# Optimization experiments

Measured on AMD Instinct MI355X. Metric: run time of the kernel, lower is better.

Reference implementation:

```python
import jax, jax.numpy as jnp
import numpy as np

B, C, H, W = 4, 512, 64, 64
C8 = C // 8


def setup_inputs() -> dict:
    key = jax.random.key(0)
    ks = jax.random.split(key, 8)
    s = 0.02
    return {
        "x": jax.random.normal(ks[0], (B, C, H, W), dtype=jnp.float32),
        "wq": jax.random.normal(ks[1], (C8, C), dtype=jnp.float32) * s,
        "bq": jax.random.normal(ks[2], (C8,), dtype=jnp.float32) * s,
        "wk": jax.random.normal(ks[3], (C8, C), dtype=jnp.float32) * s,
        "bk": jax.random.normal(ks[4], (C8,), dtype=jnp.float32) * s,
        "wv": jax.random.normal(ks[5], (C, C), dtype=jnp.float32) * s,
        "bv": jax.random.normal(ks[6], (C,), dtype=jnp.float32) * s,
        "gamma": jax.random.normal(ks[7], (1,), dtype=jnp.float32),
    }


def reference(x, wq, bq, wk, bk, wv, bv, gamma):
    b, c, h, w = x.shape
    # 1x1 convs == per-pixel linear projections
    q = jnp.einsum('bchw,oc->bohw', x, wq) + bq[None, :, None, None]  # [B,C8,H,W]
    k = jnp.einsum('bchw,oc->bohw', x, wk) + bk[None, :, None, None]  # [B,C8,H,W]
    v = jnp.einsum('bchw,oc->bohw', x, wv) + bv[None, :, None, None]  # [B,C,H,W]
    qf = q.reshape(b, c // 8, h * w)  # [B,C8,HW]
    kf = k.reshape(b, c // 8, h * w)  # [B,C8,HW]
    # energy[b,i,j] = q_i . k_j, viewed as [B,H,W,H,W]; softmax over last dim
    energy = jnp.einsum('bci,bcj->bij', qf, kf).reshape(b, h, w, h, w)
    attn = jax.nn.softmax(energy, axis=-1)  # [B,H,W,H2,W2]
    # torch: out = bmm(value, permute(0,1,3,2,4).view(B,HW,HW))
    # rows index (h,h2) into value's spatial grid; cols index output (w,w2)
    out = jnp.einsum('bchk,bhwkv->bcwv', v, attn)  # [B,C,H,W]
    return gamma * out + x
```

## Files before the change

kernel.cpp:

```cpp
#include <hip/hip_runtime.h>
#include <hip/hip_bf16.h>


typedef __bf16 bf16_t;
typedef __bf16 bf16x8 __attribute__((ext_vector_type(8)));
typedef __bf16 bf16x4 __attribute__((ext_vector_type(4)));
typedef float f32x4 __attribute__((ext_vector_type(4)));

#define HW_ 4096
#define CIN 512
#define CQ 64

__device__ __forceinline__ void gload16(const void* g, void* l) {
  __builtin_amdgcn_global_load_lds((const __attribute__((address_space(1))) void*)g,
                                   (__attribute__((address_space(3))) void*)l, 16, 0, 0);
}

__global__ __launch_bounds__(256) void k_wcat(const float* __restrict__ wq,
                                              const float* __restrict__ wk,
                                              const float* __restrict__ wv,
                                              bf16_t* __restrict__ Wcat) {
  int idx = (blockIdx.x * 256 + threadIdx.x) * 4;
  int row = idx >> 9, c = idx & 511;
  const float* src;
  if (row < 64)       src = wq + row * 512 + c;
  else if (row < 128) src = wk + (row - 64) * 512 + c;
  else                src = wv + (row - 128) * 512 + c;
  float4 v = *(const float4*)src;
  bf16x4 o = { (bf16_t)v.x, (bf16_t)v.y, (bf16_t)v.z, (bf16_t)v.w };
  *(bf16x4*)&Wcat[idx] = o;
}

__global__ __launch_bounds__(256) void k_prep(const float* __restrict__ x, bf16_t* __restrict__ xT) {
  __shared__ float tile[64][65];
  const int b = blockIdx.z;
  const int p0 = blockIdx.x * 64, c0 = blockIdx.y * 64;
  const float* xb = x + (size_t)b * CIN * HW_;
  bf16_t* xTb = xT + (size_t)b * HW_ * CIN;
  const int tid = threadIdx.x;
  const int r = tid >> 4, q = tid & 15;
#pragma unroll
  for (int i = 0; i < 4; ++i) {
    int lr = r + 16 * i;
    float4 v = *(const float4*)&xb[(size_t)(c0 + lr) * HW_ + p0 + q * 4];
    tile[lr][q * 4 + 0] = v.x; tile[lr][q * 4 + 1] = v.y;
    tile[lr][q * 4 + 2] = v.z; tile[lr][q * 4 + 3] = v.w;
  }
  __syncthreads();
#pragma unroll
  for (int i = 0; i < 4; ++i) {
    int pr = r + 16 * i;
    bf16x4 o;
    o[0] = (bf16_t)tile[q * 4 + 0][pr];
    o[1] = (bf16_t)tile[q * 4 + 1][pr];
    o[2] = (bf16_t)tile[q * 4 + 2][pr];
    o[3] = (bf16_t)tile[q * 4 + 3][pr];
    *(bf16x4*)&xTb[(size_t)(p0 + pr) * CIN + c0 + q * 4] = o;
  }
}

__global__ __launch_bounds__(256) void k_projqk(const bf16_t* __restrict__ Wcat,
                                                const bf16_t* __restrict__ xT,
                                                const float* __restrict__ bq,
                                                const float* __restrict__ bk,
                                                bf16_t* __restrict__ qfT,
                                                bf16_t* __restrict__ kfT) {
  __shared__ bf16_t As[128][64];
  __shared__ bf16_t Bs[128][64];
  const int b = blockIdx.z;
  const int n0 = blockIdx.x * 128;
  const char* Wb = (const char*)Wcat;
  const char* Xb = (const char*)(xT + (size_t)b * HW_ * CIN);
  const int tid = threadIdx.x, wv_ = tid >> 6, lane = tid & 63;
  const int wm = wv_ >> 1, wn = wv_ & 1;
  const int g = lane >> 4, cc = lane & 15;
  f32x4 acc[4][4]{};
  for (int ks = 0; ks < 512; ks += 64) {
    if (ks) __syncthreads();
#pragma unroll
    for (int i = 0; i < 4; ++i) {
      int ch = wv_ * 4 + i;
      int rr = ch * 8 + (lane >> 3);
      int sl = (lane & 7) ^ (rr & 7);
      gload16(Wb + (size_t)rr * 1024 + ks * 2 + sl * 16, (char*)As + ch * 1024);
      gload16(Xb + (size_t)(n0 + rr) * 1024 + ks * 2 + sl * 16, (char*)Bs + ch * 1024);
    }
    __syncthreads();
#pragma unroll
    for (int k2 = 0; k2 < 2; ++k2) {
      bf16x8 a[4], bb[4];
#pragma unroll
      for (int f = 0; f < 4; ++f)
        a[f] = *(const bf16x8*)((char*)As + (wm * 64 + f * 16 + cc) * 128 + (((k2 * 4 + g) ^ (cc & 7)) * 16));
#pragma unroll
      for (int f = 0; f < 4; ++f)
        bb[f] = *(const bf16x8*)((char*)Bs + (wn * 64 + f * 16 + cc) * 128 + (((k2 * 4 + g) ^ (cc & 7)) * 16));
#pragma unroll
      for (int fm = 0; fm < 4; ++fm)
#pragma unroll
        for (int fn = 0; fn < 4; ++fn)
          acc[fm][fn] = __builtin_amdgcn_mfma_f32_16x16x32_bf16(a[fm], bb[fn], acc[fm][fn], 0, 0, 0);
    }
  }
  bf16_t* qb = qfT + (size_t)b * HW_ * CQ;
  bf16_t* kb = kfT + (size_t)b * HW_ * CQ;
#pragma unroll
  for (int fm = 0; fm < 4; ++fm) {
#pragma unroll
    for (int j = 0; j < 4; ++j) {
      int m = wm * 64 + fm * 16 + g * 4 + j;
      float bias = (m < 64) ? bq[m] : bk[m - 64];
#pragma unroll
      for (int fn = 0; fn < 4; ++fn) {
        int n = n0 + wn * 64 + fn * 16 + cc;
        float val = acc[fm][fn][j] + bias;
        if (m < 64) qb[(size_t)n * CQ + m] = (bf16_t)val;
        else        kb[(size_t)n * CQ + (m - 64)] = (bf16_t)val;
      }
    }
  }
}

__global__ __launch_bounds__(256) void k_projv(const bf16_t* __restrict__ Wcat,
                                               const bf16_t* __restrict__ xT,
                                               const float* __restrict__ bv,
                                               bf16_t* __restrict__ Vp2) {
  __shared__ bf16_t As[128][64];
  __shared__ bf16_t Bs[128][64];
  const int b = blockIdx.z;
  const int n0 = blockIdx.x * 128, m0 = blockIdx.y * 128;
  const char* Wb = (const char*)Wcat;
  const char* Xb = (const char*)(xT + (size_t)b * HW_ * CIN);
  const int tid = threadIdx.x, wv_ = tid >> 6, lane = tid & 63;
  const int wm = wv_ >> 1, wn = wv_ & 1;
  const int g = lane >> 4, cc = lane & 15;
  f32x4 acc[4][4]{};
  for (int ks = 0; ks < 512; ks += 64) {
    if (ks) __syncthreads();
#pragma unroll
    for (int i = 0; i < 4; ++i) {
      int ch = wv_ * 4 + i;
      int rr = ch * 8 + (lane >> 3);
      int sl = (lane & 7) ^ (rr & 7);
      int pix = (rr & 63) * 64 + (blockIdx.x * 2) + (rr >> 6);
      gload16(Wb + (size_t)(128 + m0 + rr) * 1024 + ks * 2 + sl * 16, (char*)As + ch * 1024);
      gload16(Xb + (size_t)pix * 1024 + ks * 2 + sl * 16, (char*)Bs + ch * 1024);
    }
    __syncthreads();
#pragma unroll
    for (int k2 = 0; k2 < 2; ++k2) {
      bf16x8 a[4], bb[4];
#pragma unroll
      for (int f = 0; f < 4; ++f)
        a[f] = *(const bf16x8*)((char*)As + (wm * 64 + f * 16 + cc) * 128 + (((k2 * 4 + g) ^ (cc & 7)) * 16));
#pragma unroll
      for (int f = 0; f < 4; ++f)
        bb[f] = *(const bf16x8*)((char*)Bs + (wn * 64 + f * 16 + cc) * 128 + (((k2 * 4 + g) ^ (cc & 7)) * 16));
#pragma unroll
      for (int fm = 0; fm < 4; ++fm)
#pragma unroll
        for (int fn = 0; fn < 4; ++fn)
          acc[fm][fn] = __builtin_amdgcn_mfma_f32_16x16x32_bf16(a[fm], bb[fn], acc[fm][fn], 0, 0, 0);
    }
  }
  bf16_t* Vb = Vp2 + (size_t)b * CIN * HW_;
#pragma unroll
  for (int fm = 0; fm < 4; ++fm) {
#pragma unroll
    for (int j = 0; j < 4; ++j) {
      int m = m0 + wm * 64 + fm * 16 + g * 4 + j;
      float bias = bv[m];
#pragma unroll
      for (int fn = 0; fn < 4; ++fn) {
        int n = n0 + wn * 64 + fn * 16 + cc;
        Vb[(size_t)m * HW_ + n] = (bf16_t)(acc[fm][fn][j] + bias);
      }
    }
  }
}

__global__ __launch_bounds__(256) void k_energy(const bf16_t* __restrict__ qfT,
                                                const bf16_t* __restrict__ kfT,
                                                bf16_t* __restrict__ Pt, int zbase) {
  __shared__ bf16_t As[128][64];
  __shared__ bf16_t Bs[64][64];
  const int b = zbase + blockIdx.z;
  const int w0 = blockIdx.x * 2, ky = blockIdx.y;
  const char* qb = (const char*)(qfT + (size_t)b * HW_ * CQ);
  const char* kb = (const char*)(kfT + (size_t)b * HW_ * CQ);
  bf16_t* Ptb = Pt + (size_t)blockIdx.z * 16777216;
  const int tid = threadIdx.x, wv_ = tid >> 6, lane = tid & 63;
  const int g = lane >> 4, cc = lane & 15;
  f32x4 acc[2][4]{};
#pragma unroll
  for (int i = 0; i < 4; ++i) {
    int ch = wv_ * 4 + i;
    int rr = ch * 8 + (lane >> 3);
    int sl = (lane & 7) ^ (rr & 7);
    int pix = (rr & 63) * 64 + w0 + (rr >> 6);
    gload16(qb + (size_t)pix * 128 + sl * 16, (char*)As + ch * 1024);
  }
#pragma unroll
  for (int i = 0; i < 2; ++i) {
    int ch = wv_ * 2 + i;
    int rr = ch * 8 + (lane >> 3);
    int sl = (lane & 7) ^ (rr & 7);
    gload16(kb + (size_t)(ky * 64 + rr) * 128 + sl * 16, (char*)Bs + ch * 1024);
  }
  __syncthreads();
#pragma unroll
  for (int k2 = 0; k2 < 2; ++k2) {
    bf16x8 a[2], bb[4];
#pragma unroll
    for (int f = 0; f < 2; ++f)
      a[f] = *(const bf16x8*)((char*)As + (wv_ * 32 + f * 16 + cc) * 128 + (((k2 * 4 + g) ^ (cc & 7)) * 16));
#pragma unroll
    for (int f = 0; f < 4; ++f)
      bb[f] = *(const bf16x8*)((char*)Bs + (f * 16 + cc) * 128 + (((k2 * 4 + g) ^ (cc & 7)) * 16));
#pragma unroll
    for (int fm = 0; fm < 2; ++fm)
#pragma unroll
      for (int fn = 0; fn < 4; ++fn)
        acc[fm][fn] = __builtin_amdgcn_mfma_f32_16x16x32_bf16(a[fm], bb[fn], acc[fm][fn], 0, 0, 0);
  }
  const int w = w0 + (wv_ >> 1);
#pragma unroll
  for (int fm = 0; fm < 2; ++fm) {
    float e[4][4], invj[4];
#pragma unroll
    for (int j = 0; j < 4; ++j) {
      float mx = fmaxf(fmaxf(acc[fm][0][j], acc[fm][1][j]), fmaxf(acc[fm][2][j], acc[fm][3][j]));
#pragma unroll
      for (int d = 1; d < 16; d <<= 1) mx = fmaxf(mx, __shfl_xor(mx, d, 64));
      float s = 0.f;
#pragma unroll
      for (int fn = 0; fn < 4; ++fn) { e[fn][j] = __expf(acc[fm][fn][j] - mx); s += e[fn][j]; }
#pragma unroll
      for (int d = 1; d < 16; d <<= 1) s += __shfl_xor(s, d, 64);
      invj[j] = __builtin_amdgcn_rcpf(s);
    }
    int h0 = (wv_ & 1) * 32 + fm * 16 + g * 4;
#pragma unroll
    for (int fn = 0; fn < 4; ++fn) {
      int v = fn * 16 + cc;
      bf16x4 pk = { (bf16_t)(e[fn][0] * invj[0]), (bf16_t)(e[fn][1] * invj[1]),
                    (bf16_t)(e[fn][2] * invj[2]), (bf16_t)(e[fn][3] * invj[3]) };
      *(bf16x4*)&Ptb[(((size_t)w * 64 + ky) * 64 + v) * 64 + h0] = pk;
    }
  }
}

__global__ __launch_bounds__(256) void k_out(const bf16_t* __restrict__ Vp2,
                                             const bf16_t* __restrict__ Pt,
                                             const float* __restrict__ x,
                                             const float* __restrict__ gamma,
                                             float* __restrict__ outp, int zbase) {
  __shared__ char Ls[65536];
  const int b = zbase + blockIdx.z;
  const int c0 = blockIdx.x * 128, w0 = blockIdx.y * 2;
  const char* Vb = (const char*)(Vp2 + (size_t)b * CIN * HW_);
  const char* Pb = (const char*)(Pt + (size_t)blockIdx.z * 16777216);
  const int tid = threadIdx.x, wv_ = tid >> 6, lane = tid & 63;
  const int wm = wv_ >> 1, wn = wv_ & 1;
  const int g = lane >> 4, cc = lane & 15;

  const char* aSb[4]; const char* bSb[4];
#pragma unroll
  for (int r = 0; r < 4; ++r) {
    int L = (r * 4 + wv_) * 64 + lane;
    int arow = L >> 3, asl = (L & 7) ^ (arow & 7);
    aSb[r] = Vb + (size_t)(c0 + arow) * 8192 + asl * 16;
    int ws = L >> 9, e = L & 511, v = e >> 3, bsl = (e & 7) ^ (v & 7);
    bSb[r] = Pb + (size_t)(w0 + ws) * 524288 + v * 128 + bsl * 16;
  }
  int aoff[2][4], boff[2][4];
#pragma unroll
  for (int k2 = 0; k2 < 2; ++k2) {
#pragma unroll
    for (int fm = 0; fm < 4; ++fm)
      aoff[k2][fm] = (wm * 64 + fm * 16 + cc) * 128 + (((k2 * 4 + g) ^ (cc & 7)) * 16);
#pragma unroll
    for (int fn = 0; fn < 4; ++fn)
      boff[k2][fn] = 16384 + wn * 8192 + (fn * 16 + cc) * 128 + (((k2 * 4 + g) ^ (cc & 7)) * 16);
  }

  f32x4 acc[4][4]{};
  {
    char* base = Ls;
#pragma unroll
    for (int r = 0; r < 4; ++r) gload16(aSb[r], base + (r * 4 + wv_) * 1024);
#pragma unroll
    for (int r = 0; r < 4; ++r) gload16(bSb[r], base + 16384 + (r * 4 + wv_) * 1024);
  }
  for (int s = 0; s < 64; ++s) {
    if (s < 63) {
      char* base = Ls + ((s + 1) & 1) * 32768;
#pragma unroll
      for (int r = 0; r < 4; ++r) gload16(aSb[r] + (size_t)(s + 1) * 128, base + (r * 4 + wv_) * 1024);
#pragma unroll
      for (int r = 0; r < 4; ++r) gload16(bSb[r] + (size_t)(s + 1) * 8192, base + 16384 + (r * 4 + wv_) * 1024);
      asm volatile("s_waitcnt vmcnt(8)" ::: "memory");
    } else {
      asm volatile("s_waitcnt vmcnt(0)" ::: "memory");
    }
    __builtin_amdgcn_s_barrier();
    const char* base = Ls + (s & 1) * 32768;
#pragma unroll
    for (int k2 = 0; k2 < 2; ++k2) {
      bf16x8 a[4], bb[4];
#pragma unroll
      for (int fm = 0; fm < 4; ++fm) a[fm] = *(const bf16x8*)(base + aoff[k2][fm]);
#pragma unroll
      for (int fn = 0; fn < 4; ++fn) bb[fn] = *(const bf16x8*)(base + boff[k2][fn]);
#pragma unroll
      for (int fm = 0; fm < 4; ++fm)
#pragma unroll
        for (int fn = 0; fn < 4; ++fn)
          acc[fm][fn] = __builtin_amdgcn_mfma_f32_16x16x32_bf16(a[fm], bb[fn], acc[fm][fn], 0, 0, 0);
    }
    asm volatile("s_waitcnt lgkmcnt(0)" ::: "memory");
    __builtin_amdgcn_s_barrier();
  }
  const float gmm = gamma[0];
  const float* xb = x + (size_t)b * CIN * HW_;
  float* ob = outp + (size_t)b * CIN * HW_;
  const int w = w0 + wn;
#pragma unroll
  for (int fm = 0; fm < 4; ++fm) {
#pragma unroll
    for (int jj = 0; jj < 4; ++jj) {
      int c = c0 + wm * 64 + fm * 16 + g * 4 + jj;
#pragma unroll
      for (int fn = 0; fn < 4; ++fn) {
        int n = w * 64 + fn * 16 + cc;
        size_t idx = (size_t)c * HW_ + n;
        ob[idx] = gmm * acc[fm][fn][jj] + xb[idx];
      }
    }
  }
}

extern "C" void kernel_launch(void* const* d_in, const int* in_sizes, int n_in,
                              void* d_out, int out_size, void* d_ws, size_t ws_size,
                              hipStream_t stream) {
  const float* x  = (const float*)d_in[0];
  const float* wq = (const float*)d_in[1];
  const float* bq = (const float*)d_in[2];
  const float* wk = (const float*)d_in[3];
  const float* bk = (const float*)d_in[4];
  const float* wv = (const float*)d_in[5];
  const float* bv = (const float*)d_in[6];
  const float* gamma = (const float*)d_in[7];
  float* outp = (float*)d_out;
  char* ws = (char*)d_ws;
  size_t off = 0;
  bf16_t* xT   = (bf16_t*)(ws + off); off += (size_t)4 * HW_ * CIN * 2;
  bf16_t* Wcat = (bf16_t*)(ws + off); off += (size_t)640 * CIN * 2;
  bf16_t* qfT  = (bf16_t*)(ws + off); off += (size_t)4 * HW_ * CQ * 2;
  bf16_t* kfT  = (bf16_t*)(ws + off); off += (size_t)4 * HW_ * CQ * 2;
  bf16_t* Vp2  = (bf16_t*)(ws + off); off += (size_t)4 * CIN * HW_ * 2;
  bf16_t* Pt   = (bf16_t*)(ws + off);
  const size_t pbytes = (size_t)HW_ * HW_ * 2;
  const bool full = (ws_size >= off + 4 * pbytes);

  k_wcat<<<dim3(320), dim3(256), 0, stream>>>(wq, wk, wv, Wcat);
  k_prep<<<dim3(64, 8, 4), dim3(256), 0, stream>>>(x, xT);
  k_projqk<<<dim3(32, 1, 4), dim3(256), 0, stream>>>(Wcat, xT, bq, bk, qfT, kfT);
  k_projv<<<dim3(32, 4, 4), dim3(256), 0, stream>>>(Wcat, xT, bv, Vp2);
  if (full) {
    k_energy<<<dim3(32, 64, 4), dim3(256), 0, stream>>>(qfT, kfT, Pt, 0);
    k_out<<<dim3(4, 32, 4), dim3(256), 0, stream>>>(Vp2, Pt, x, gamma, outp, 0);
  } else {
    for (int b = 0; b < 4; ++b) {
      k_energy<<<dim3(32, 64, 1), dim3(256), 0, stream>>>(qfT, kfT, Pt, b);
      k_out<<<dim3(4, 32, 1), dim3(256), 0, stream>>>(Vp2, Pt, x, gamma, outp, b);
    }
  }
}
```

Before: 190.7 us.

## Load attention B-fragments directly into registers in k_out, halve LDS footprint

The output GEMM kernel no longer stages the attention-probability (B) tiles through shared memory. Each wave now loads its B fragments straight from global memory into registers, double-buffered across two register sets. Only the V (A) tile still goes through LDS, which halves shared memory to 32KB, and launch bounds now request 3 blocks per SM for more occupancy. In exchange, register pressure rises, the global B loads lose the swizzled LDS reuse between waves that share a wn, and the vmcnt accounting gets more fragile.

```diff
diff --git a/kernel.cpp b/kernel.cpp
--- a/kernel.cpp
+++ b/kernel.cpp
@@ -250,12 +250,39 @@
   }
 }
 
-__global__ __launch_bounds__(256) void k_out(const bf16_t* __restrict__ Vp2,
-                                             const bf16_t* __restrict__ Pt,
-                                             const float* __restrict__ x,
-                                             const float* __restrict__ gamma,
-                                             float* __restrict__ outp, int zbase) {
-  __shared__ char Ls[65536];
+#define LOADB(dst, base) do {                              \
+    dst[0] = *(const bf16x8*)((base));                     \
+    dst[1] = *(const bf16x8*)((base) + 64);                \
+    dst[2] = *(const bf16x8*)((base) + 2048);              \
+    dst[3] = *(const bf16x8*)((base) + 2112);              \
+    dst[4] = *(const bf16x8*)((base) + 4096);              \
+    dst[5] = *(const bf16x8*)((base) + 4160);              \
+    dst[6] = *(const bf16x8*)((base) + 6144);              \
+    dst[7] = *(const bf16x8*)((base) + 6208);              \
+  } while (0)
+
+#define COMPUTE(lbase, breg) do {                                                                  \
+    _Pragma("unroll")                                                                              \
+    for (int k2 = 0; k2 < 2; ++k2) {                                                               \
+      bf16x8 afr[4];                                                                               \
+      _Pragma("unroll")                                                                            \
+      for (int fm = 0; fm < 4; ++fm) afr[fm] = *(const bf16x8*)((lbase) + aoff[k2][fm]);           \
+      _Pragma("unroll")                                                                            \
+      for (int fm = 0; fm < 4; ++fm) {                                                             \
+        acc[fm][0] = __builtin_amdgcn_mfma_f32_16x16x32_bf16(afr[fm], breg[k2],     acc[fm][0], 0, 0, 0); \
+        acc[fm][1] = __builtin_amdgcn_mfma_f32_16x16x32_bf16(afr[fm], breg[2 + k2], acc[fm][1], 0, 0, 0); \
+        acc[fm][2] = __builtin_amdgcn_mfma_f32_16x16x32_bf16(afr[fm], breg[4 + k2], acc[fm][2], 0, 0, 0); \
+        acc[fm][3] = __builtin_amdgcn_mfma_f32_16x16x32_bf16(afr[fm], breg[6 + k2], acc[fm][3], 0, 0, 0); \
+      }                                                                                            \
+    }                                                                                              \
+  } while (0)
+
+__global__ __launch_bounds__(256, 3) void k_out(const bf16_t* __restrict__ Vp2,
+                                                const bf16_t* __restrict__ Pt,
+                                                const float* __restrict__ x,
+                                                const float* __restrict__ gamma,
+                                                float* __restrict__ outp, int zbase) {
+  __shared__ char As2[32768];
   const int b = zbase + blockIdx.z;
   const int c0 = blockIdx.x * 128, w0 = blockIdx.y * 2;
   const char* Vb = (const char*)(Vp2 + (size_t)b * CIN * HW_);
@@ -264,62 +291,59 @@
   const int wm = wv_ >> 1, wn = wv_ & 1;
   const int g = lane >> 4, cc = lane & 15;
 
-  const char* aSb[4]; const char* bSb[4];
+  const char* aSb[4];
+  char* aD0[4]; char* aD1[4];
 #pragma unroll
   for (int r = 0; r < 4; ++r) {
     int L = (r * 4 + wv_) * 64 + lane;
     int arow = L >> 3, asl = (L & 7) ^ (arow & 7);
     aSb[r] = Vb + (size_t)(c0 + arow) * 8192 + asl * 16;
-    int ws = L >> 9, e = L & 511, v = e >> 3, bsl = (e & 7) ^ (v & 7);
-    bSb[r] = Pb + (size_t)(w0 + ws) * 524288 + v * 128 + bsl * 16;
-  }
-  int aoff[2][4], boff[2][4];
-#pragma unroll
-  for (int k2 = 0; k2 < 2; ++k2) {
+    aD0[r] = As2 + (r * 4 + wv_) * 1024;
+    aD1[r] = aD0[r] + 16384;
+  }
+  int aoff[2][4];
+#pragma unroll
+  for (int k2 = 0; k2 < 2; ++k2)
 #pragma unroll
     for (int fm = 0; fm < 4; ++fm)
       aoff[k2][fm] = (wm * 64 + fm * 16 + cc) * 128 + (((k2 * 4 + g) ^ (cc & 7)) * 16);
-#pragma unroll
-    for (int fn = 0; fn < 4; ++fn)
-      boff[k2][fn] = 16384 + wn * 8192 + (fn * 16 + cc) * 128 + (((k2 * 4 + g) ^ (cc & 7)) * 16);
-  }
+
+  const char* bB = Pb + (size_t)(w0 + wn) * 524288 + (size_t)cc * 128 + g * 16;
 
   f32x4 acc[4][4]{};
-  {
-    char* base = Ls;
-#pragma unroll
-    for (int r = 0; r < 4; ++r) gload16(aSb[r], base + (r * 4 + wv_) * 1024);
-#pragma unroll
-    for (int r = 0; r < 4; ++r) gload16(bSb[r], base + 16384 + (r * 4 + wv_) * 1024);
-  }
-  for (int s = 0; s < 64; ++s) {
-    if (s < 63) {
-      char* base = Ls + ((s + 1) & 1) * 32768;
-#pragma unroll
-      for (int r = 0; r < 4; ++r) gload16(aSb[r] + (size_t)(s + 1) * 128, base + (r * 4 + wv_) * 1024);
-#pragma unroll
-      for (int r = 0; r < 4; ++r) gload16(bSb[r] + (size_t)(s + 1) * 8192, base + 16384 + (r * 4 + wv_) * 1024);
-      asm volatile("s_waitcnt vmcnt(8)" ::: "memory");
-    } else {
-      asm volatile("s_waitcnt vmcnt(0)" ::: "memory");
-    }
-    __builtin_amdgcn_s_barrier();
-    const char* base = Ls + (s & 1) * 32768;
-#pragma unroll
-    for (int k2 = 0; k2 < 2; ++k2) {
-      bf16x8 a[4], bb[4];
-#pragma unroll
-      for (int fm = 0; fm < 4; ++fm) a[fm] = *(const bf16x8*)(base + aoff[k2][fm]);
-#pragma unroll
-      for (int fn = 0; fn < 4; ++fn) bb[fn] = *(const bf16x8*)(base + boff[k2][fn]);
-#pragma unroll
-      for (int fm = 0; fm < 4; ++fm)
-#pragma unroll
-        for (int fn = 0; fn < 4; ++fn)
-          acc[fm][fn] = __builtin_amdgcn_mfma_f32_16x16x32_bf16(a[fm], bb[fn], acc[fm][fn], 0, 0, 0);
-    }
-    asm volatile("s_waitcnt lgkmcnt(0)" ::: "memory");
-    __builtin_amdgcn_s_barrier();
+  bf16x8 b0[8], b1[8];
+#pragma unroll
+  for (int r = 0; r < 4; ++r) gload16(aSb[r], aD0[r]);
+  LOADB(b0, bB);
+
+  for (int s2 = 0; s2 < 32; ++s2) {
+    {
+#pragma unroll
+      for (int r = 0; r < 4; ++r) gload16(aSb[r] + (size_t)(2 * s2 + 1) * 128, aD1[r]);
+      const char* q = bB + 8192;
+      LOADB(b1, q);
+      asm volatile("s_waitcnt vmcnt(12)" ::: "memory");
+      __builtin_amdgcn_s_barrier();
+      COMPUTE(As2, b0);
+      asm volatile("s_waitcnt lgkmcnt(0)" ::: "memory");
+      __builtin_amdgcn_s_barrier();
+    }
+    {
+      if (s2 < 31) {
+#pragma unroll
+        for (int r = 0; r < 4; ++r) gload16(aSb[r] + (size_t)(2 * s2 + 2) * 128, aD0[r]);
+        const char* q = bB + 16384;
+        LOADB(b0, q);
+        asm volatile("s_waitcnt vmcnt(12)" ::: "memory");
+      } else {
+        asm volatile("s_waitcnt vmcnt(0)" ::: "memory");
+      }
+      __builtin_amdgcn_s_barrier();
+      COMPUTE(As2 + 16384, b1);
+      asm volatile("s_waitcnt lgkmcnt(0)" ::: "memory");
+      __builtin_amdgcn_s_barrier();
+      bB += 16384;
+    }
   }
   const float gmm = gamma[0];
   const float* xb = x + (size_t)b * CIN * HW_;
```

Measured after the change: 240.1 us. +25.9%, slower.
